# Performance work log

Measured on AMD Instinct MI355X. Metric: run time of the kernel, lower is better.

Reference implementation:

```python
import jax, jax.numpy as jnp
import numpy as np
from jax import lax

N = 64          # n (even -> odd=0, add_odd=0)
B = 256         # batch
F = 256         # input_features
ITERS = 10      # sinkhorn iterations


def _conv1d(x, w, b, pad, dil):
    # x: (B, Cin, L), w: (Cout, Cin, K) torch layout
    y = lax.conv_general_dilated(
        x, w, window_strides=(1,), padding=[(pad, pad)],
        rhs_dilation=(dil,), dimension_numbers=("NCH", "OIH", "NCH"))
    return y + b[None, :, None]


def setup_inputs() -> dict:
    key = jax.random.key(0)
    ks = jax.random.split(key, 17)
    s = 0.02
    d = {
        "x": jax.random.normal(ks[0], (B, F), jnp.float32),
        # linear stack (torch Linear layout: (out, in))
        "w1": jax.random.normal(ks[1], (2 * N, F), jnp.float32) * s,
        "b1": jax.random.normal(ks[2], (2 * N,), jnp.float32) * s,
        "w2": jax.random.normal(ks[3], (N * N, 2 * N), jnp.float32) * s,
        "b2": jax.random.normal(ks[4], (N * N,), jnp.float32) * s,
        "w3": jax.random.normal(ks[5], (4 * N * N, N * N), jnp.float32) * s,
        "b3": jax.random.normal(ks[6], (4 * N * N,), jnp.float32) * s,
        # conv stack: 2n->3n->2n->n->n->n, all k=3
        "cw1": jax.random.normal(ks[7], (3 * N, 2 * N, 3), jnp.float32) * s,
        "cb1": jax.random.normal(ks[8], (3 * N,), jnp.float32) * s,
        "cw2": jax.random.normal(ks[9], (2 * N, 3 * N, 3), jnp.float32) * s,
        "cb2": jax.random.normal(ks[10], (2 * N,), jnp.float32) * s,
        "cw3": jax.random.normal(ks[11], (N, 2 * N, 3), jnp.float32) * s,
        "cb3": jax.random.normal(ks[12], (N,), jnp.float32) * s,
        "cw4": jax.random.normal(ks[13], (N, N, 3), jnp.float32) * s,
        "cb4": jax.random.normal(ks[14], (N,), jnp.float32) * s,
        "cw5": jax.random.normal(ks[15], (N, N, 3), jnp.float32) * s,
        "cb5": jax.random.normal(ks[16], (N,), jnp.float32) * s,
    }
    return d


def _sink(x, iters):
    # output = x + 0.001; repeat: row-normalize then col-normalize
    out = x + 0.001

    def body(o, _):
        o = o / jnp.sum(o, axis=2, keepdims=True)  # row_sink: divide each row by its sum
        o = o / jnp.sum(o, axis=1, keepdims=True)  # col_sink: divide each column by its sum
        return o, None

    out, _ = lax.scan(body, out, None, length=iters)
    return out


def reference(x, w1, b1, w2, b2, w3, b3,
              cw1, cb1, cw2, cb2, cw3, cb3, cw4, cb4, cw5, cb5):
    h = x @ w1.T + b1
    h = h @ w2.T + b2
    h = h @ w3.T + b3                      # (B, 4n^2)
    h = h.reshape(B, 2 * N, 2 * N)         # (B, 128, 128)
    # conv1: p=0, d=(n-8)//2=28 (since n>10); rest pad=0, dil=1
    h = _conv1d(h, cw1, cb1, 0, (N - 8) // 2)  # (B, 192, 72)
    h = _conv1d(h, cw2, cb2, 0, 1)             # (B, 128, 70)
    h = _conv1d(h, cw3, cb3, 0, 1)             # (B, 64, 68)
    h = _conv1d(h, cw4, cb4, 0, 1)             # (B, 64, 66)
    h = _conv1d(h, cw5, cb5, 0, 1)             # (B, 64, 64)
    h = h * h                                   # torch.pow(x, 2)
    return _sink(h, ITERS)
```

## Files before the change

### kernel.cpp

```cpp
#include <hip/hip_runtime.h>
#include <hip/hip_bf16.h>

typedef float f32x4 __attribute__((ext_vector_type(4)));
typedef __bf16 bf16x8 __attribute__((ext_vector_type(8)));

typedef __attribute__((address_space(1))) const unsigned int as1_uint;
typedef __attribute__((address_space(3))) unsigned int as3_uint;

__global__ __launch_bounds__(128) void gemm1_k(const float* __restrict__ x,
                                               const float* __restrict__ w1,
                                               const float* __restrict__ b1,
                                               float* __restrict__ h1) {
    __shared__ float xs[256];
    const int m = blockIdx.x, t = threadIdx.x;
    xs[t] = x[m * 256 + t];
    xs[t + 128] = x[m * 256 + 128 + t];
    __syncthreads();
    float acc = b1[t];
    const float4* wr = (const float4*)(w1 + t * 256);
#pragma unroll 8
    for (int k4 = 0; k4 < 64; ++k4) {
        float4 w = wr[k4];
        acc += xs[k4 * 4 + 0] * w.x + xs[k4 * 4 + 1] * w.y +
               xs[k4 * 4 + 2] * w.z + xs[k4 * 4 + 3] * w.w;
    }
    h1[m * 128 + t] = acc;
}

__global__ __launch_bounds__(256) void gemm2_k(const float* __restrict__ h1,
                                               const float* __restrict__ w2,
                                               const float* __restrict__ b2,
                                               char* __restrict__ h2b) {
    __shared__ float As[64][129];
    __shared__ float Bs[64][129];
    const int nb = blockIdx.x, mb = blockIdx.y, t = threadIdx.x;
#pragma unroll
    for (int i = 0; i < 8; ++i) {
        int idx = i * 256 + t;
        int row = idx >> 5, c4 = (idx & 31) * 4;
        float4 a = *(const float4*)(h1 + (mb * 64 + row) * 128 + c4);
        As[row][c4 + 0] = a.x; As[row][c4 + 1] = a.y;
        As[row][c4 + 2] = a.z; As[row][c4 + 3] = a.w;
        float4 bv = *(const float4*)(w2 + (nb * 64 + row) * 128 + c4);
        Bs[row][c4 + 0] = bv.x; Bs[row][c4 + 1] = bv.y;
        Bs[row][c4 + 2] = bv.z; Bs[row][c4 + 3] = bv.w;
    }
    __syncthreads();
    const int tx = t & 15, ty = t >> 4;
    float acc[4][4] = {};
#pragma unroll 4
    for (int k = 0; k < 128; ++k) {
        float a[4], b[4];
#pragma unroll
        for (int i = 0; i < 4; ++i) a[i] = As[ty * 4 + i][k];
#pragma unroll
        for (int j = 0; j < 4; ++j) b[j] = Bs[tx * 4 + j][k];
#pragma unroll
        for (int i = 0; i < 4; ++i)
#pragma unroll
            for (int j = 0; j < 4; ++j) acc[i][j] += a[i] * b[j];
    }
#pragma unroll
    for (int i = 0; i < 4; ++i)
#pragma unroll
        for (int j = 0; j < 4; ++j) {
            int m = mb * 64 + ty * 4 + i;
            int n = nb * 64 + tx * 4 + j;
            float v = acc[i][j] + b2[n];
            int kb = n >> 6, r = n & 63;
            int byte = kb * 32768 + ((m * 128 + (r >> 3) * 16) ^ ((m & 7) << 4)) + (r & 7) * 2;
            *(__bf16*)(h2b + byte) = (__bf16)v;
        }
}

__global__ __launch_bounds__(512, 1) void gemm3_k(const char* __restrict__ Ab,
                                                  const float* __restrict__ W,
                                                  char* __restrict__ parts) {
    __shared__ __align__(16) char lds[81920];
    const int tid = threadIdx.x;
    const int nb = blockIdx.x >> 1, ks = blockIdx.x & 1;
    const int n0 = nb * 64;
    const int lane = tid & 63, wid = tid >> 6;
    const int mrow = tid >> 3, kb8 = tid & 7;

#define ISSUE_A(kt, buf)                                                            \
    {                                                                               \
        const char* _s = Ab + (kt) * 32768 + wid * 4096 + lane * 16;                \
        char* _d = lds + (buf) * 32768 + wid * 4096;                                \
        __builtin_amdgcn_global_load_lds((as1_uint*)(_s), (as3_uint*)(_d), 16, 0, 0);             \
        __builtin_amdgcn_global_load_lds((as1_uint*)(_s + 1024), (as3_uint*)(_d + 1024), 16, 0, 0); \
        __builtin_amdgcn_global_load_lds((as1_uint*)(_s + 2048), (as3_uint*)(_d + 2048), 16, 0, 0); \
        __builtin_amdgcn_global_load_lds((as1_uint*)(_s + 3072), (as3_uint*)(_d + 3072), 16, 0, 0); \
    }

    float4 w0r, w1r;
    auto loadW = [&](int kt) {
        const float* q = W + (n0 + mrow) * 4096 + kt * 64 + kb8 * 8;
        w0r = *(const float4*)q;
        w1r = *(const float4*)(q + 4);
    };
    auto storeW = [&](int buf) {
        bf16x8 p;
        p[0] = (__bf16)w0r.x; p[1] = (__bf16)w0r.y; p[2] = (__bf16)w0r.z; p[3] = (__bf16)w0r.w;
        p[4] = (__bf16)w1r.x; p[5] = (__bf16)w1r.y; p[6] = (__bf16)w1r.z; p[7] = (__bf16)w1r.w;
        *(bf16x8*)(lds + 65536 + buf * 8192 +
                   ((mrow * 128 + kb8 * 16) ^ ((mrow & 7) << 4))) = p;
    };

    const int kt0 = ks * 32;

    ISSUE_A(kt0, 0);
    loadW(kt0);
    __syncthreads();
    storeW(0);
    __syncthreads();

    const int lr = lane & 15, lq = lane >> 4;
    const int wm = wid >> 1, wn = wid & 1;

    f32x4 acc[4][2];
    const f32x4 zero = {0.f, 0.f, 0.f, 0.f};
#pragma unroll
    for (int mi = 0; mi < 4; ++mi)
#pragma unroll
        for (int ni = 0; ni < 2; ++ni) acc[mi][ni] = zero;

    for (int t = 0; t < 32; ++t) {
        const int cur = t & 1;
        if (t < 31) {
            ISSUE_A(kt0 + t + 1, cur ^ 1);
            loadW(kt0 + t + 1);
        }
        const char* Ac = lds + cur * 32768;
        const char* Wc = lds + 65536 + cur * 8192;
#pragma unroll
        for (int kk = 0; kk < 2; ++kk) {
            const int kb = kk * 4 + lq;
            bf16x8 af[4], bfv[2];
#pragma unroll
            for (int mi = 0; mi < 4; ++mi) {
                int m = wm * 64 + mi * 16 + lr;
                af[mi] = *(const bf16x8*)(Ac + ((m * 128 + kb * 16) ^ ((m & 7) << 4)));
            }
#pragma unroll
            for (int ni = 0; ni < 2; ++ni) {
                int n = wn * 32 + ni * 16 + lr;
                bfv[ni] = *(const bf16x8*)(Wc + ((n * 128 + kb * 16) ^ ((n & 7) << 4)));
            }
#pragma unroll
            for (int mi = 0; mi < 4; ++mi)
#pragma unroll
                for (int ni = 0; ni < 2; ++ni)
                    acc[mi][ni] = __builtin_amdgcn_mfma_f32_16x16x32_bf16(
                        af[mi], bfv[ni], acc[mi][ni], 0, 0, 0);
        }
        __syncthreads();
        if (t < 31) storeW(cur ^ 1);
        __syncthreads();
    }
#undef ISSUE_A

    __bf16* P = (__bf16*)(parts + ks * 8388608);
#pragma unroll
    for (int mi = 0; mi < 4; ++mi)
#pragma unroll
        for (int ni = 0; ni < 2; ++ni) {
            const int n = n0 + wn * 32 + ni * 16 + lr;
#pragma unroll
            for (int r = 0; r < 4; ++r) {
                int m = wm * 64 + mi * 16 + lq * 4 + r;
                P[m * 16384 + n] = (__bf16)acc[mi][ni][r];
            }
        }
}

template <int CIN, int COUT, int DIL, int MT, int NT>
__device__ __forceinline__ void conv_core(const char* xt, char* wl,
                                          const float* __restrict__ w,
                                          f32x4 (&acc)[MT][NT], int tid) {
    constexpr int RB = CIN * 2;
    const int lane = tid & 63, wid = tid >> 6;
    const int lr = lane & 15, lq = lane >> 4;
    const int cobase = wid * (COUT / 4);
    const f32x4 zero = {0.f, 0.f, 0.f, 0.f};
#pragma unroll
    for (int mi = 0; mi < MT; ++mi)
#pragma unroll
        for (int ni = 0; ni < NT; ++ni) acc[mi][ni] = zero;

    for (int cic = 0; cic < CIN / 32; ++cic) {
        for (int idx = tid; idx < COUT * 4; idx += 256) {
            int co = idx >> 2, cib = idx & 3, ci0 = cic * 32 + cib * 8;
            const float* src = w + co * (CIN * 3) + ci0 * 3;
            float v[24];
#pragma unroll
            for (int u = 0; u < 6; ++u) {
                float4 f = *(const float4*)(src + u * 4);
                v[u * 4 + 0] = f.x; v[u * 4 + 1] = f.y;
                v[u * 4 + 2] = f.z; v[u * 4 + 3] = f.w;
            }
#pragma unroll
            for (int tp = 0; tp < 3; ++tp) {
                bf16x8 pk;
#pragma unroll
                for (int j = 0; j < 8; ++j) pk[j] = (__bf16)v[j * 3 + tp];
                *(bf16x8*)(wl + ((tp * 4 + cib) * COUT + co) * 16) = pk;
            }
        }
        __syncthreads();
#pragma unroll
        for (int tp = 0; tp < 3; ++tp) {
            bf16x8 af[MT];
#pragma unroll
            for (int mi = 0; mi < MT; ++mi)
                af[mi] = *(const bf16x8*)(wl + ((tp * 4 + lq) * COUT + cobase + mi * 16 + lr) * 16);
            bf16x8 bfr[NT];
#pragma unroll
            for (int ni = 0; ni < NT; ++ni) {
                int colX = ni * 16 + lr + tp * DIL;
                bfr[ni] = *(const bf16x8*)(xt + ((colX * RB + (cic * 4 + lq) * 16) ^ ((colX & 7) << 4)));
            }
#pragma unroll
            for (int mi = 0; mi < MT; ++mi)
#pragma unroll
                for (int ni = 0; ni < NT; ++ni)
                    acc[mi][ni] = __builtin_amdgcn_mfma_f32_16x16x32_bf16(
                        af[mi], bfr[ni], acc[mi][ni], 0, 0, 0);
        }
        __syncthreads();
    }
}

template <int COUT, int LOUT, int MT, int NT>
__device__ __forceinline__ void write_xt(char* xt_out, const f32x4 (&acc)[MT][NT],
                                         const float* __restrict__ bias, int tid) {
    constexpr int RBO = COUT * 2;
    const int lane = tid & 63, wid = tid >> 6;
    const int lr = lane & 15, lq = lane >> 4;
    const int cobase = wid * (COUT / 4);
#pragma unroll
    for (int mi = 0; mi < MT; ++mi)
#pragma unroll
        for (int ni = 0; ni < NT; ++ni) {
            int l = ni * 16 + lr;
            if (l < LOUT) {
#pragma unroll
                for (int r = 0; r < 4; ++r) {
                    int co = cobase + mi * 16 + lq * 4 + r;
                    float y = acc[mi][ni][r] + bias[co];
                    int byte = (l * RBO + ((co >> 3) << 4) + (co & 7) * 2) ^ ((l & 7) << 4);
                    *(__bf16*)(xt_out + byte) = (__bf16)y;
                }
            }
        }
}

__global__ __launch_bounds__(256, 1) void convsink_k(
    const char* __restrict__ parts, const float* __restrict__ b3,
    const float* __restrict__ cw1, const float* __restrict__ cb1,
    const float* __restrict__ cw2, const float* __restrict__ cb2,
    const float* __restrict__ cw3, const float* __restrict__ cb3,
    const float* __restrict__ cw4, const float* __restrict__ cb4,
    const float* __restrict__ cw5, const float* __restrict__ cb5,
    float* __restrict__ out) {
    __shared__ __align__(16) char lds[34816 + 31488 + 36864 + 16640];
    char* xtA = lds;
    char* xtB = lds + 34816;
    char* wl = lds + 34816 + 31488;
    float* S = (float*)(lds + 34816 + 31488 + 36864);

    const int b = blockIdx.x, tid = threadIdx.x;
    const __bf16* p0 = (const __bf16*)parts + (size_t)b * 16384;
    const __bf16* p1 = (const __bf16*)(parts + 8388608) + (size_t)b * 16384;

#pragma unroll
    for (int i = 0; i < 8; ++i) {
        int idx = i * 256 + tid;
        int l = idx & 127, cib = idx >> 7;
        bf16x8 p;
#pragma unroll
        for (int j = 0; j < 8; ++j) {
            int n = (cib * 8 + j) * 128 + l;
            float v = (float)p0[n] + (float)p1[n] + b3[n];
            p[j] = (__bf16)v;
        }
        *(bf16x8*)(xtA + ((l * 256 + cib * 16) ^ ((l & 7) << 4))) = p;
    }
    __syncthreads();

    {
        f32x4 acc[3][5];
        conv_core<128, 192, 28, 3, 5>(xtA, wl, cw1, acc, tid);
        write_xt<192, 72, 3, 5>(xtB, acc, cb1, tid);
    }
    __syncthreads();
    {
        f32x4 acc[2][5];
        conv_core<192, 128, 1, 2, 5>(xtB, wl, cw2, acc, tid);
        write_xt<128, 70, 2, 5>(xtA, acc, cb2, tid);
    }
    __syncthreads();
    {
        f32x4 acc[1][5];
        conv_core<128, 64, 1, 1, 5>(xtA, wl, cw3, acc, tid);
        write_xt<64, 68, 1, 5>(xtB, acc, cb3, tid);
    }
    __syncthreads();
    {
        f32x4 acc[1][5];
        conv_core<64, 64, 1, 1, 5>(xtB, wl, cw4, acc, tid);
        write_xt<64, 66, 1, 5>(xtA, acc, cb4, tid);
    }
    __syncthreads();
    {
        f32x4 acc[1][4];
        conv_core<64, 64, 1, 1, 4>(xtA, wl, cw5, acc, tid);
        const int lane = tid & 63, wid = tid >> 6;
        const int lr = lane & 15, lq = lane >> 4;
        const int cobase = wid * 16;
#pragma unroll
        for (int ni = 0; ni < 4; ++ni) {
            int l = ni * 16 + lr;
#pragma unroll
            for (int r = 0; r < 4; ++r) {
                int co = cobase + lq * 4 + r;
                float y = acc[0][ni][r] + cb5[co];
                S[co * 65 + l] = y * y + 0.001f;
            }
        }
    }
    __syncthreads();

    const int q = tid & 3, rid = tid >> 2;
    for (int it = 0; it < 10; ++it) {
        float p = 0.f;
#pragma unroll
        for (int j = 0; j < 16; ++j) p += S[rid * 65 + q * 16 + j];
        p += __shfl_xor(p, 1);
        p += __shfl_xor(p, 2);
        float inv = 1.0f / p;
#pragma unroll
        for (int j = 0; j < 16; ++j) S[rid * 65 + q * 16 + j] *= inv;
        __syncthreads();
        float c = 0.f;
#pragma unroll
        for (int i = 0; i < 16; ++i) c += S[(q * 16 + i) * 65 + rid];
        c += __shfl_xor(c, 1);
        c += __shfl_xor(c, 2);
        float invc = 1.0f / c;
#pragma unroll
        for (int i = 0; i < 16; ++i) S[(q * 16 + i) * 65 + rid] *= invc;
        __syncthreads();
    }

#pragma unroll
    for (int i = 0; i < 16; ++i) {
        int idx = i * 256 + tid;
        out[b * 4096 + idx] = S[(idx >> 6) * 65 + (idx & 63)];
    }
}

extern "C" void kernel_launch(void* const* d_in, const int* in_sizes, int n_in,
                              void* d_out, int out_size, void* d_ws, size_t ws_size,
                              hipStream_t stream) {
    const float* x = (const float*)d_in[0];
    const float* w1 = (const float*)d_in[1];
    const float* b1 = (const float*)d_in[2];
    const float* w2 = (const float*)d_in[3];
    const float* b2 = (const float*)d_in[4];
    const float* w3 = (const float*)d_in[5];
    const float* b3 = (const float*)d_in[6];
    const float* cw1 = (const float*)d_in[7];
    const float* cb1 = (const float*)d_in[8];
    const float* cw2 = (const float*)d_in[9];
    const float* cb2 = (const float*)d_in[10];
    const float* cw3 = (const float*)d_in[11];
    const float* cb3 = (const float*)d_in[12];
    const float* cw4 = (const float*)d_in[13];
    const float* cb4 = (const float*)d_in[14];
    const float* cw5 = (const float*)d_in[15];
    const float* cb5 = (const float*)d_in[16];
    float* out = (float*)d_out;

    char* ws = (char*)d_ws;
    float* h1 = (float*)(ws);
    char* h2b = ws + 131072;
    char* parts = ws + 131072 + 2097152;

    gemm1_k<<<256, 128, 0, stream>>>(x, w1, b1, h1);
    gemm2_k<<<dim3(64, 4), 256, 0, stream>>>(h1, w2, b2, h2b);
    gemm3_k<<<512, 512, 0, stream>>>(h2b, w3, parts);
    convsink_k<<<256, 256, 0, stream>>>(parts, b3, cw1, cb1, cw2, cb2,
                                        cw3, cb3, cw4, cb4, cw5, cb5, out);
}
```

Baseline: 131.2 us.

## Deepen gemm3 W prefetch to two stages with manual waitcnt and one barrier per step

Restructures the gemm3 main loop so W is prefetched two tiles ahead into alternating register sets, while A is still loaded asynchronously into LDS. The loop now uses explicit vmcnt/lgkmcnt waits and a single s_barrier per step instead of two __syncthreads. The goal is to hide global W load latency and cut barrier overhead. In exchange it adds register pressure and depends on hand-counted waitcnt values, which must match the number of outstanding loads to stay correct.

```diff
diff --git a/kernel.cpp b/kernel.cpp
--- a/kernel.cpp
+++ b/kernel.cpp
@@ -82,6 +82,11 @@
     const int n0 = nb * 64;
     const int lane = tid & 63, wid = tid >> 6;
     const int mrow = tid >> 3, kb8 = tid & 7;
+    const int kt0 = ks * 32;
+    const int lr = lane & 15, lq = lane >> 4;
+    const int wm = wid >> 1, wn = wid & 1;
+
+    const float* Wlane = W + (size_t)(n0 + mrow) * 4096 + kb8 * 8;
 
 #define ISSUE_A(kt, buf)                                                            \
     {                                                                               \
@@ -93,31 +98,21 @@
         __builtin_amdgcn_global_load_lds((as1_uint*)(_s + 3072), (as3_uint*)(_d + 3072), 16, 0, 0); \
     }
 
-    float4 w0r, w1r;
-    auto loadW = [&](int kt) {
-        const float* q = W + (n0 + mrow) * 4096 + kt * 64 + kb8 * 8;
-        w0r = *(const float4*)q;
-        w1r = *(const float4*)(q + 4);
-    };
-    auto storeW = [&](int buf) {
+#define LOADW(d0, d1, kt)                                 \
+    {                                                     \
+        const float* _q = Wlane + (size_t)(kt) * 64;      \
+        d0 = *(const float4*)_q;                          \
+        d1 = *(const float4*)(_q + 4);                    \
+    }
+
+    auto storeW2 = [&](const float4& a, const float4& b, int buf) {
         bf16x8 p;
-        p[0] = (__bf16)w0r.x; p[1] = (__bf16)w0r.y; p[2] = (__bf16)w0r.z; p[3] = (__bf16)w0r.w;
-        p[4] = (__bf16)w1r.x; p[5] = (__bf16)w1r.y; p[6] = (__bf16)w1r.z; p[7] = (__bf16)w1r.w;
+        p[0] = (__bf16)a.x; p[1] = (__bf16)a.y; p[2] = (__bf16)a.z; p[3] = (__bf16)a.w;
+        p[4] = (__bf16)b.x; p[5] = (__bf16)b.y; p[6] = (__bf16)b.z; p[7] = (__bf16)b.w;
         *(bf16x8*)(lds + 65536 + buf * 8192 +
                    ((mrow * 128 + kb8 * 16) ^ ((mrow & 7) << 4))) = p;
     };
 
-    const int kt0 = ks * 32;
-
-    ISSUE_A(kt0, 0);
-    loadW(kt0);
-    __syncthreads();
-    storeW(0);
-    __syncthreads();
-
-    const int lr = lane & 15, lq = lane >> 4;
-    const int wm = wid >> 1, wn = wid & 1;
-
     f32x4 acc[4][2];
     const f32x4 zero = {0.f, 0.f, 0.f, 0.f};
 #pragma unroll
@@ -125,14 +120,7 @@
 #pragma unroll
         for (int ni = 0; ni < 2; ++ni) acc[mi][ni] = zero;
 
-    for (int t = 0; t < 32; ++t) {
-        const int cur = t & 1;
-        if (t < 31) {
-            ISSUE_A(kt0 + t + 1, cur ^ 1);
-            loadW(kt0 + t + 1);
-        }
-        const char* Ac = lds + cur * 32768;
-        const char* Wc = lds + 65536 + cur * 8192;
+    auto mfma_tile = [&](const char* Ac, const char* Wc) {
 #pragma unroll
         for (int kk = 0; kk < 2; ++kk) {
             const int kb = kk * 4 + lq;
@@ -154,10 +142,53 @@
                     acc[mi][ni] = __builtin_amdgcn_mfma_f32_16x16x32_bf16(
                         af[mi], bfv[ni], acc[mi][ni], 0, 0, 0);
         }
-        __syncthreads();
-        if (t < 31) storeW(cur ^ 1);
-        __syncthreads();
-    }
+    };
+
+    float4 wE0, wE1, wO0, wO1;
+
+    LOADW(wE0, wE1, kt0);
+    ISSUE_A(kt0, 0);
+    storeW2(wE0, wE1, 0);
+    LOADW(wO0, wO1, kt0 + 1);
+    asm volatile("s_waitcnt vmcnt(2)" ::: "memory");
+    __builtin_amdgcn_sched_barrier(0);
+    asm volatile("s_waitcnt lgkmcnt(0)" ::: "memory");
+    __builtin_amdgcn_sched_barrier(0);
+    __builtin_amdgcn_s_barrier();
+
+#define G3_STEP(tt, CUR, WS0, WS1, WL0, WL1)                                   \
+    {                                                                          \
+        ISSUE_A(kt0 + (tt) + 1, (CUR) ^ 1);                                    \
+        LOADW(WL0, WL1, kt0 + (tt) + 2);                                       \
+        __builtin_amdgcn_sched_barrier(0);                                     \
+        mfma_tile(lds + (CUR) * 32768, lds + 65536 + (CUR) * 8192);            \
+        storeW2(WS0, WS1, (CUR) ^ 1);                                          \
+        asm volatile("s_waitcnt vmcnt(2)" ::: "memory");                       \
+        __builtin_amdgcn_sched_barrier(0);                                     \
+        asm volatile("s_waitcnt lgkmcnt(0)" ::: "memory");                     \
+        __builtin_amdgcn_sched_barrier(0);                                     \
+        __builtin_amdgcn_s_barrier();                                          \
+    }
+
+#pragma unroll 1
+    for (int i = 0; i < 15; ++i) {
+        G3_STEP(2 * i, 0, wO0, wO1, wE0, wE1);
+        G3_STEP(2 * i + 1, 1, wE0, wE1, wO0, wO1);
+    }
+    {
+        ISSUE_A(kt0 + 31, 1);
+        mfma_tile(lds, lds + 65536);
+        storeW2(wO0, wO1, 1);
+        asm volatile("s_waitcnt vmcnt(0)" ::: "memory");
+        __builtin_amdgcn_sched_barrier(0);
+        asm volatile("s_waitcnt lgkmcnt(0)" ::: "memory");
+        __builtin_amdgcn_sched_barrier(0);
+        __builtin_amdgcn_s_barrier();
+    }
+    mfma_tile(lds + 32768, lds + 65536 + 8192);
+
+#undef G3_STEP
+#undef LOADW
 #undef ISSUE_A
 
     __bf16* P = (__bf16*)(parts + ks * 8388608);
```

Result: no change. 132.2 us (+0.8%).

## Read A fragments directly from global in gemm3, shrink LDS for occupancy

Applied to the files above, without the earlier changes.

gemm3 stops staging the activation tile A in LDS through global_load_lds and has each lane read its bf16x8 A fragments straight from global memory. gemm2 now writes h2b unswizzled so those direct reads are contiguous. LDS falls from 80KB to 16KB, holding only the double-buffered W tile, and launch bounds rise to 4 blocks per CU so more waves can hide latency. In exchange, A fragments are re-read from global/L2 by each wave rather than shared through LDS, and a global-load latency now sits on the MFMA path.

```diff
diff --git a/kernel.cpp b/kernel.cpp
--- a/kernel.cpp
+++ b/kernel.cpp
@@ -3,9 +3,6 @@
 
 typedef float f32x4 __attribute__((ext_vector_type(4)));
 typedef __bf16 bf16x8 __attribute__((ext_vector_type(8)));
-
-typedef __attribute__((address_space(1))) const unsigned int as1_uint;
-typedef __attribute__((address_space(3))) unsigned int as3_uint;
 
 __global__ __launch_bounds__(128) void gemm1_k(const float* __restrict__ x,
                                                const float* __restrict__ w1,
@@ -68,56 +65,40 @@
             int n = nb * 64 + tx * 4 + j;
             float v = acc[i][j] + b2[n];
             int kb = n >> 6, r = n & 63;
-            int byte = kb * 32768 + ((m * 128 + (r >> 3) * 16) ^ ((m & 7) << 4)) + (r & 7) * 2;
+            int byte = kb * 32768 + m * 128 + (r >> 3) * 16 + (r & 7) * 2;
             *(__bf16*)(h2b + byte) = (__bf16)v;
         }
 }
 
-__global__ __launch_bounds__(512, 1) void gemm3_k(const char* __restrict__ Ab,
+__global__ __launch_bounds__(512, 4) void gemm3_k(const char* __restrict__ Ab,
                                                   const float* __restrict__ W,
                                                   char* __restrict__ parts) {
-    __shared__ __align__(16) char lds[81920];
+    __shared__ __align__(16) char lds[16384];
     const int tid = threadIdx.x;
     const int nb = blockIdx.x >> 1, ks = blockIdx.x & 1;
     const int n0 = nb * 64;
     const int lane = tid & 63, wid = tid >> 6;
     const int mrow = tid >> 3, kb8 = tid & 7;
-
-#define ISSUE_A(kt, buf)                                                            \
-    {                                                                               \
-        const char* _s = Ab + (kt) * 32768 + wid * 4096 + lane * 16;                \
-        char* _d = lds + (buf) * 32768 + wid * 4096;                                \
-        __builtin_amdgcn_global_load_lds((as1_uint*)(_s), (as3_uint*)(_d), 16, 0, 0);             \
-        __builtin_amdgcn_global_load_lds((as1_uint*)(_s + 1024), (as3_uint*)(_d + 1024), 16, 0, 0); \
-        __builtin_amdgcn_global_load_lds((as1_uint*)(_s + 2048), (as3_uint*)(_d + 2048), 16, 0, 0); \
-        __builtin_amdgcn_global_load_lds((as1_uint*)(_s + 3072), (as3_uint*)(_d + 3072), 16, 0, 0); \
-    }
-
-    float4 w0r, w1r;
-    auto loadW = [&](int kt) {
-        const float* q = W + (n0 + mrow) * 4096 + kt * 64 + kb8 * 8;
-        w0r = *(const float4*)q;
-        w1r = *(const float4*)(q + 4);
+    const int kt0 = ks * 32;
+    const int lr = lane & 15, lq = lane >> 4;
+    const int wm = wid >> 1, wn = wid & 1;
+
+    const float* Wlane = W + (size_t)(n0 + mrow) * 4096 + kb8 * 8;
+    const char* Abase = Ab + (wm * 64 + lr) * 128 + lq * 16;
+
+    auto loadW = [&](int kt, float4& d0, float4& d1) {
+        const float* q = Wlane + (size_t)kt * 64;
+        d0 = *(const float4*)q;
+        d1 = *(const float4*)(q + 4);
     };
-    auto storeW = [&](int buf) {
+    auto storeW2 = [&](const float4& a, const float4& b, int buf) {
         bf16x8 p;
-        p[0] = (__bf16)w0r.x; p[1] = (__bf16)w0r.y; p[2] = (__bf16)w0r.z; p[3] = (__bf16)w0r.w;
-        p[4] = (__bf16)w1r.x; p[5] = (__bf16)w1r.y; p[6] = (__bf16)w1r.z; p[7] = (__bf16)w1r.w;
-        *(bf16x8*)(lds + 65536 + buf * 8192 +
+        p[0] = (__bf16)a.x; p[1] = (__bf16)a.y; p[2] = (__bf16)a.z; p[3] = (__bf16)a.w;
+        p[4] = (__bf16)b.x; p[5] = (__bf16)b.y; p[6] = (__bf16)b.z; p[7] = (__bf16)b.w;
+        *(bf16x8*)(lds + buf * 8192 +
                    ((mrow * 128 + kb8 * 16) ^ ((mrow & 7) << 4))) = p;
     };
 
-    const int kt0 = ks * 32;
-
-    ISSUE_A(kt0, 0);
-    loadW(kt0);
-    __syncthreads();
-    storeW(0);
-    __syncthreads();
-
-    const int lr = lane & 15, lq = lane >> 4;
-    const int wm = wid >> 1, wn = wid & 1;
-
     f32x4 acc[4][2];
     const f32x4 zero = {0.f, 0.f, 0.f, 0.f};
 #pragma unroll
@@ -125,27 +106,18 @@
 #pragma unroll
         for (int ni = 0; ni < 2; ++ni) acc[mi][ni] = zero;
 
-    for (int t = 0; t < 32; ++t) {
-        const int cur = t & 1;
-        if (t < 31) {
-            ISSUE_A(kt0 + t + 1, cur ^ 1);
-            loadW(kt0 + t + 1);
-        }
-        const char* Ac = lds + cur * 32768;
-        const char* Wc = lds + 65536 + cur * 8192;
+    auto mfma_tile = [&](int kt, const char* Wc) {
+        const char* Ak = Abase + (size_t)kt * 32768;
 #pragma unroll
         for (int kk = 0; kk < 2; ++kk) {
-            const int kb = kk * 4 + lq;
             bf16x8 af[4], bfv[2];
 #pragma unroll
-            for (int mi = 0; mi < 4; ++mi) {
-                int m = wm * 64 + mi * 16 + lr;
-                af[mi] = *(const bf16x8*)(Ac + ((m * 128 + kb * 16) ^ ((m & 7) << 4)));
-            }
+            for (int mi = 0; mi < 4; ++mi)
+                af[mi] = *(const bf16x8*)(Ak + mi * 2048 + kk * 64);
 #pragma unroll
             for (int ni = 0; ni < 2; ++ni) {
                 int n = wn * 32 + ni * 16 + lr;
-                bfv[ni] = *(const bf16x8*)(Wc + ((n * 128 + kb * 16) ^ ((n & 7) << 4)));
+                bfv[ni] = *(const bf16x8*)(Wc + ((n * 128 + (kk * 4 + lq) * 16) ^ ((n & 7) << 4)));
             }
 #pragma unroll
             for (int mi = 0; mi < 4; ++mi)
@@ -154,11 +126,23 @@
                     acc[mi][ni] = __builtin_amdgcn_mfma_f32_16x16x32_bf16(
                         af[mi], bfv[ni], acc[mi][ni], 0, 0, 0);
         }
-        __syncthreads();
-        if (t < 31) storeW(cur ^ 1);
-        __syncthreads();
-    }
-#undef ISSUE_A
+    };
+
+    float4 wc0, wc1;
+    loadW(kt0, wc0, wc1);
+    storeW2(wc0, wc1, 0);
+    __syncthreads();
+
+#pragma unroll 1
+    for (int t = 0; t < 32; ++t) {
+        const int cur = t & 1;
+        float4 wn0, wn1;
+        if (t < 31) loadW(kt0 + t + 1, wn0, wn1);
+        mfma_tile(kt0 + t, lds + cur * 8192);
+        __syncthreads();
+        if (t < 31) storeW2(wn0, wn1, cur ^ 1);
+        __syncthreads();
+    }
 
     __bf16* P = (__bf16*)(parts + ks * 8388608);
 #pragma unroll
```

New measurement: 209.3 us. 1.6x slower.

## Write gemm3 partials in swizzled conv layout and fold bias into gemm3

Applied to the files above, without the earlier changes.

gemm3 now adds the b3 bias (on the first K-split only) and writes each partial result directly in the swizzled channel-major bf16 layout that the conv kernel's LDS expects. The conv kernel can then fetch both partial images with direct global-to-LDS loads and sum them with 16-byte vector ops, replacing the old scalar gathered bf16 loads and bias reads. The cost moves to gemm3's epilogue, whose scattered 2-byte stores become less coalesced. xtB grows to 32 KB so it can hold a full partial image.

```diff
diff --git a/kernel.cpp b/kernel.cpp
--- a/kernel.cpp
+++ b/kernel.cpp
@@ -75,6 +75,7 @@
 
 __global__ __launch_bounds__(512, 1) void gemm3_k(const char* __restrict__ Ab,
                                                   const float* __restrict__ W,
+                                                  const float* __restrict__ b3,
                                                   char* __restrict__ parts) {
     __shared__ __align__(16) char lds[81920];
     const int tid = threadIdx.x;
@@ -95,7 +96,7 @@
 
     float4 w0r, w1r;
     auto loadW = [&](int kt) {
-        const float* q = W + (n0 + mrow) * 4096 + kt * 64 + kb8 * 8;
+        const float* q = W + (size_t)(n0 + mrow) * 4096 + kt * 64 + kb8 * 8;
         w0r = *(const float4*)q;
         w1r = *(const float4*)(q + 4);
     };
@@ -160,18 +161,21 @@
     }
 #undef ISSUE_A
 
-    __bf16* P = (__bf16*)(parts + ks * 8388608);
-#pragma unroll
-    for (int mi = 0; mi < 4; ++mi)
-#pragma unroll
-        for (int ni = 0; ni < 2; ++ni) {
-            const int n = n0 + wn * 32 + ni * 16 + lr;
+    char* P = parts + (size_t)ks * 8388608;
+#pragma unroll
+    for (int ni = 0; ni < 2; ++ni) {
+        const int n = n0 + wn * 32 + ni * 16 + lr;
+        const int ci = n >> 7, l = n & 127;
+        const int cibyte = ((l * 256 + (ci >> 3) * 16) ^ ((l & 7) << 4)) + (ci & 7) * 2;
+        const float bv = (ks == 0) ? b3[n] : 0.0f;
+#pragma unroll
+        for (int mi = 0; mi < 4; ++mi)
 #pragma unroll
             for (int r = 0; r < 4; ++r) {
                 int m = wm * 64 + mi * 16 + lq * 4 + r;
-                P[m * 16384 + n] = (__bf16)acc[mi][ni][r];
-            }
-        }
+                *(__bf16*)(P + (size_t)m * 32768 + cibyte) = (__bf16)(acc[mi][ni][r] + bv);
+            }
+    }
 }
 
 template <int CIN, int COUT, int DIL, int MT, int NT>
@@ -256,35 +260,43 @@
 }
 
 __global__ __launch_bounds__(256, 1) void convsink_k(
-    const char* __restrict__ parts, const float* __restrict__ b3,
+    const char* __restrict__ parts,
     const float* __restrict__ cw1, const float* __restrict__ cb1,
     const float* __restrict__ cw2, const float* __restrict__ cb2,
     const float* __restrict__ cw3, const float* __restrict__ cb3,
     const float* __restrict__ cw4, const float* __restrict__ cb4,
     const float* __restrict__ cw5, const float* __restrict__ cb5,
     float* __restrict__ out) {
-    __shared__ __align__(16) char lds[34816 + 31488 + 36864 + 16640];
+    __shared__ __align__(16) char lds[34816 + 32768 + 36864 + 16640];
     char* xtA = lds;
     char* xtB = lds + 34816;
-    char* wl = lds + 34816 + 31488;
-    float* S = (float*)(lds + 34816 + 31488 + 36864);
+    char* wl = lds + 34816 + 32768;
+    float* S = (float*)(lds + 34816 + 32768 + 36864);
 
     const int b = blockIdx.x, tid = threadIdx.x;
-    const __bf16* p0 = (const __bf16*)parts + (size_t)b * 16384;
-    const __bf16* p1 = (const __bf16*)(parts + 8388608) + (size_t)b * 16384;
+    const int lane = tid & 63, wid = tid >> 6;
+    const char* img0 = parts + (size_t)b * 32768;
+    const char* img1 = parts + 8388608 + (size_t)b * 32768;
 
 #pragma unroll
     for (int i = 0; i < 8; ++i) {
-        int idx = i * 256 + tid;
-        int l = idx & 127, cib = idx >> 7;
-        bf16x8 p;
-#pragma unroll
-        for (int j = 0; j < 8; ++j) {
-            int n = (cib * 8 + j) * 128 + l;
-            float v = (float)p0[n] + (float)p1[n] + b3[n];
-            p[j] = (__bf16)v;
-        }
-        *(bf16x8*)(xtA + ((l * 256 + cib * 16) ^ ((l & 7) << 4))) = p;
+        const int off = wid * 1024 + i * 4096;
+        __builtin_amdgcn_global_load_lds((as1_uint*)(img0 + off + lane * 16),
+                                         (as3_uint*)(xtA + off), 16, 0, 0);
+        __builtin_amdgcn_global_load_lds((as1_uint*)(img1 + off + lane * 16),
+                                         (as3_uint*)(xtB + off), 16, 0, 0);
+    }
+    __syncthreads();
+
+#pragma unroll
+    for (int i = 0; i < 8; ++i) {
+        int off = i * 4096 + tid * 16;
+        bf16x8 a = *(const bf16x8*)(xtA + off);
+        bf16x8 c = *(const bf16x8*)(xtB + off);
+        bf16x8 s;
+#pragma unroll
+        for (int j = 0; j < 8; ++j) s[j] = (__bf16)((float)a[j] + (float)c[j]);
+        *(bf16x8*)(xtA + off) = s;
     }
     __syncthreads();
 
@@ -315,7 +327,6 @@
     {
         f32x4 acc[1][4];
         conv_core<64, 64, 1, 1, 4>(xtA, wl, cw5, acc, tid);
-        const int lane = tid & 63, wid = tid >> 6;
         const int lr = lane & 15, lq = lane >> 4;
         const int cobase = wid * 16;
 #pragma unroll
@@ -389,7 +400,7 @@
 
     gemm1_k<<<256, 128, 0, stream>>>(x, w1, b1, h1);
     gemm2_k<<<dim3(64, 4), 256, 0, stream>>>(h1, w2, b2, h2b);
-    gemm3_k<<<512, 512, 0, stream>>>(h2b, w3, parts);
-    convsink_k<<<256, 256, 0, stream>>>(parts, b3, cw1, cb1, cw2, cb2,
+    gemm3_k<<<512, 512, 0, stream>>>(h2b, w3, b3, parts);
+    convsink_k<<<256, 256, 0, stream>>>(parts, cw1, cb1, cw2, cb2,
                                         cw3, cb3, cw4, cb4, cw5, cb5, out);
 }
```

After: 155.5 us. +18.6%, slower.
